# Performance work log

Hardware: AMD Instinct MI355X
Metric: run time of the kernel (lower is better)

Reference implementation:

```python
import jax, jax.numpy as jnp
import numpy as np


def setup_inputs() -> dict:
    key = jax.random.key(0)
    k1, k2, k3, k4 = jax.random.split(key, 4)
    B, D_vis, E, N = 512, 4096, 1024, 512
    vf = jax.random.normal(k1, (B, D_vis), dtype=jnp.float32)
    p_lfs = jax.random.normal(k2, (B, E), dtype=jnp.float32)
    n_lfs = jax.random.normal(k3, (N, E), dtype=jnp.float32)
    W = jax.random.normal(k4, (E, D_vis), dtype=jnp.float32) * (1.0 / np.sqrt(D_vis))
    b = jnp.zeros((E,), dtype=jnp.float32)
    return {"vf": vf, "p_lfs": p_lfs, "n_lfs": n_lfs, "W": W, "b": b}


def _partial_order_sim(hypers, hypos):
    # -||relu(hypers - hypos)||_2 along last dim
    act = jax.nn.relu(hypers - hypos)
    return -jnp.sqrt(jnp.sum(act * act, axis=-1))


def reference(vf, p_lfs, n_lfs, W, b):
    # vf: [B, D_vis], W: [E, D_vis] -> vf_emb: [B, E]
    vf_emb = jnp.einsum("bd,ed->be", vf, W) + b
    # positive scores: [B]
    p_scores = _partial_order_sim(p_lfs, vf_emb)
    # negative scores, batched over B: n_lfs [N,E] vs vf_emb [B,E] -> [B,N]
    n_scores = _partial_order_sim(n_lfs[None, :, :], vf_emb[:, None, :])
    # score_stack: [B, 1+N]
    return jnp.concatenate([p_scores[:, None], n_scores], axis=1)
```

## Files before the change

kernel.cpp:

```cpp
#include <hip/hip_runtime.h>
#include <hip/hip_bf16.h>

constexpr int B = 512;
constexpr int D = 4096;
constexpr int E = 1024;
constexpr int N = 512;
constexpr int KS = 16;
constexpr int KC = D / KS;
constexpr int NSTEP = KC / 32;
constexpr int ES = 8;
constexpr int EC = E / ES;
constexpr int DEPTH = 2;

typedef __attribute__((ext_vector_type(8))) short bf16x8;
typedef __attribute__((ext_vector_type(4))) float f32x4;
typedef _Float16 h2 __attribute__((ext_vector_type(2)));
typedef _Float16 h4 __attribute__((ext_vector_type(4)));
typedef _Float16 h8 __attribute__((ext_vector_type(8)));

typedef __attribute__((address_space(3))) void lds_void;
typedef const __attribute__((address_space(1))) void gbl_void;

__device__ __forceinline__ unsigned short f2bf(float f) {
    __hip_bfloat16 h = __float2bfloat16(f);
    return *reinterpret_cast<unsigned short*>(&h);
}

#if __has_builtin(__builtin_amdgcn_fdot2)
__device__ __forceinline__ float fdot2(h2 a, h2 b, float c) {
    return __builtin_amdgcn_fdot2(a, b, c, false);
}
#else
__device__ __forceinline__ float fdot2(h2 a, h2 b, float c) {
    return c + (float)a[0] * (float)b[0] + (float)a[1] * (float)b[1];
}
#endif

__global__ __launch_bounds__(256) void cvt_all(
    const float* __restrict__ vf, const float* __restrict__ W,
    const float* __restrict__ n_lfs,
    unsigned short* __restrict__ vfB, unsigned short* __restrict__ WB,
    _Float16* __restrict__ n16)
{
    const int bid = blockIdx.x;
    if (bid < 3072) {
        const float* src;
        unsigned short* dst;
        int i;
        if (bid < 1024) { src = vf; dst = vfB; i = (bid * 256 + threadIdx.x) * 8; }
        else           { src = W;  dst = WB;  i = ((bid - 1024) * 256 + threadIdx.x) * 8; }
        float4 v0 = *(const float4*)(src + i);
        float4 v1 = *(const float4*)(src + i + 4);
        bf16x8 o;
        o[0] = (short)f2bf(v0.x); o[1] = (short)f2bf(v0.y);
        o[2] = (short)f2bf(v0.z); o[3] = (short)f2bf(v0.w);
        o[4] = (short)f2bf(v1.x); o[5] = (short)f2bf(v1.y);
        o[6] = (short)f2bf(v1.z); o[7] = (short)f2bf(v1.w);
        *(bf16x8*)(dst + i) = o;
    } else {
        const int i = ((bid - 3072) * 256 + threadIdx.x) * 8;
        float4 v0 = *(const float4*)(n_lfs + i);
        float4 v1 = *(const float4*)(n_lfs + i + 4);
        h8 o;
        o[0] = (_Float16)v0.x; o[1] = (_Float16)v0.y;
        o[2] = (_Float16)v0.z; o[3] = (_Float16)v0.w;
        o[4] = (_Float16)v1.x; o[5] = (_Float16)v1.y;
        o[6] = (_Float16)v1.z; o[7] = (_Float16)v1.w;
        *(h8*)(n16 + i) = o;
    }
}

__global__ __launch_bounds__(64) void gemm_lds(
    const unsigned short* __restrict__ vf,
    const unsigned short* __restrict__ W,
    _Float16* __restrict__ part)
{
    __shared__ __align__(16) char smem[17664];

    const int L  = threadIdx.x;

    const int id = blockIdx.x + 16 * blockIdx.y + 128 * blockIdx.z;
    const int l  = (id & 7) * 256 + (id >> 3);
    const int ks = l >> 7;
    const int n0 = (l & 15) * 64;
    const int m0 = ((l >> 4) & 7) * 64;

    const int subrow = L >> 2;
    const int qstg = (L & 3) ^ ((L >> 2) & 3) ^ ((L >> 4) & 3);
    const int kbeg = ks * KC;
    const unsigned short* aSrc[4];
    const unsigned short* bSrc[4];
    #pragma unroll
    for (int c = 0; c < 4; ++c) {
        aSrc[c] = vf + (size_t)(m0 + c * 16 + subrow) * D + kbeg + qstg * 8;
        bSrc[c] = W  + (size_t)(n0 + c * 16 + subrow) * D + kbeg + qstg * 8;
    }

    const int r16 = L & 15;
    const int quad = L >> 4;
    const int swz = quad ^ (r16 & 3) ^ ((r16 >> 2) & 3);
    const int aoff = r16 * 64 + swz * 16;

    f32x4 acc[4][4] = {};

    auto issue = [&](int step, int buf) {
        const size_t koff = (size_t)step * 32;
        #pragma unroll
        for (int c = 0; c < 4; ++c) {
            __builtin_amdgcn_global_load_lds(
                (gbl_void*)(aSrc[c] + koff),
                (lds_void*)(smem + buf * 4096 + c * 1024), 16, 0, 0);
            __builtin_amdgcn_global_load_lds(
                (gbl_void*)(bSrc[c] + koff),
                (lds_void*)(smem + 8192 + buf * 4096 + c * 1024), 16, 0, 0);
        }
    };

    issue(0, 0);
    issue(1, 1);

    #define GSTEP(S, WC, ISS)                                                  \
    {                                                                          \
        const int buf_ = (S) & 1;                                              \
        __builtin_amdgcn_s_waitcnt(WC);                                        \
        bf16x8 af[4], bg[4];                                                   \
        _Pragma("unroll")                                                      \
        for (int i = 0; i < 4; ++i)                                            \
            af[i] = *(const bf16x8*)(smem + buf_ * 4096 + i * 1024 + aoff);    \
        _Pragma("unroll")                                                      \
        for (int j = 0; j < 4; ++j)                                            \
            bg[j] = *(const bf16x8*)(smem + 8192 + buf_ * 4096 + j * 1024 + aoff); \
        _Pragma("unroll")                                                      \
        for (int i = 0; i < 4; ++i)                                            \
            _Pragma("unroll")                                                  \
            for (int j = 0; j < 4; ++j)                                        \
                acc[i][j] = __builtin_amdgcn_mfma_f32_16x16x32_bf16(           \
                    af[i], bg[j], acc[i][j], 0, 0, 0);                         \
        if (ISS) issue((S) + DEPTH, buf_);                                     \
    }

    #pragma unroll 1
    for (int s = 0; s < NSTEP - 1; ++s)
        GSTEP(s, 0x0F78, s + DEPTH < NSTEP);
    GSTEP(NSTEP - 1, 0x0F70, false);
    #undef GSTEP

    float* ct = (float*)smem;
    #pragma unroll
    for (int i = 0; i < 4; ++i)
        #pragma unroll
        for (int j = 0; j < 4; ++j)
            #pragma unroll
            for (int r = 0; r < 4; ++r)
                ct[(i * 16 + quad * 4 + r) * 69 + (j * 16 + r16)] = acc[i][j][r];
    __builtin_amdgcn_s_waitcnt(0xC07F);
    __builtin_amdgcn_sched_barrier(0);
    _Float16* po = part + (size_t)ks * B * E + (size_t)(m0 + L) * E + n0;
    const float* crow = ct + L * 69;
    #pragma unroll
    for (int c8 = 0; c8 < 8; ++c8) {
        h8 v;
        #pragma unroll
        for (int u = 0; u < 8; ++u) v[u] = (_Float16)crow[c8 * 8 + u];
        *(h8*)(po + c8 * 8) = v;
    }
}

__global__ __launch_bounds__(256) void reduce_emb(
    const _Float16* __restrict__ part, const float* __restrict__ bias,
    const float* __restrict__ p_lfs,
    _Float16* __restrict__ emb16, float* __restrict__ out)
{
    const int b = blockIdx.x;
    const int e = threadIdx.x * 4;
    const size_t base = (size_t)b * E + e;
    float4 s = *(const float4*)(bias + e);
    #pragma unroll
    for (int ks = 0; ks < KS; ++ks) {
        h4 p = *(const h4*)(part + (size_t)ks * B * E + base);
        s.x += (float)p[0]; s.y += (float)p[1];
        s.z += (float)p[2]; s.w += (float)p[3];
    }
    h4 o;
    o[0] = (_Float16)s.x; o[1] = (_Float16)s.y;
    o[2] = (_Float16)s.z; o[3] = (_Float16)s.w;
    *(h4*)(emb16 + base) = o;

    const float4 pl = *(const float4*)(p_lfs + base);
    float d, a = 0.f;
    d = pl.x - s.x; d = fmaxf(d, 0.f); a = fmaf(d, d, a);
    d = pl.y - s.y; d = fmaxf(d, 0.f); a = fmaf(d, d, a);
    d = pl.z - s.z; d = fmaxf(d, 0.f); a = fmaf(d, d, a);
    d = pl.w - s.w; d = fmaxf(d, 0.f); a = fmaf(d, d, a);
    #pragma unroll
    for (int off = 32; off; off >>= 1) a += __shfl_down(a, off, 64);
    __shared__ float red[4];
    if ((threadIdx.x & 63) == 0) red[threadIdx.x >> 6] = a;
    __syncthreads();
    if (threadIdx.x == 0)
        out[(size_t)b * 513] = -sqrtf(red[0] + red[1] + red[2] + red[3]);
}

__global__ __launch_bounds__(256, 4) void scores_part(
    const _Float16* __restrict__ emb16,
    const _Float16* __restrict__ n16,
    _Float16* __restrict__ pn)
{
    constexpr int LDH = EC + 8;
    __shared__ _Float16 eS[64 * LDH];
    __shared__ _Float16 nS[64 * LDH];

    const int t  = threadIdx.x;
    const int n0 = blockIdx.x * 64;
    const int b0 = blockIdx.y * 64;
    const int e0 = blockIdx.z * EC;

    {
        const int row = t >> 2;
        const int cb  = (t & 3) * 32;
        const _Float16* ep = emb16 + (size_t)(b0 + row) * E + e0 + cb;
        const _Float16* np = n16   + (size_t)(n0 + row) * E + e0 + cb;
        _Float16* ed = &eS[row * LDH + cb];
        _Float16* nd = &nS[row * LDH + cb];
        #pragma unroll
        for (int q = 0; q < 4; ++q) {
            h8 v = *(const h8*)(ep + q * 8);
            h8 w = *(const h8*)(np + q * 8);
            *(h8*)(ed + q * 8) = -v;
            *(h8*)(nd + q * 8) = w;
        }
    }
    __syncthreads();

    const int ty = t >> 4;
    const int tx = t & 15;

    float acc[4][4] = {};
    const h4 z4 = {};

    #pragma unroll 2
    for (int e = 0; e < EC; e += 4) {
        h4 a[4], c[4];
        #pragma unroll
        for (int r = 0; r < 4; ++r)
            a[r] = *(const h4*)&eS[(ty + 16 * r) * LDH + e];
        #pragma unroll
        for (int q = 0; q < 4; ++q)
            c[q] = *(const h4*)&nS[(tx + 16 * q) * LDH + e];
        #pragma unroll
        for (int r = 0; r < 4; ++r)
            #pragma unroll
            for (int q = 0; q < 4; ++q) {
                h4 d = c[q] + a[r];
                d = __builtin_elementwise_max(d, z4);
                h2 dl = __builtin_shufflevector(d, d, 0, 1);
                h2 dh = __builtin_shufflevector(d, d, 2, 3);
                acc[r][q] = fdot2(dl, dl, acc[r][q]);
                acc[r][q] = fdot2(dh, dh, acc[r][q]);
            }
    }

    _Float16* po = pn + (size_t)blockIdx.z * B * N;
    #pragma unroll
    for (int r = 0; r < 4; ++r) {
        const size_t ob = (size_t)(b0 + ty + 16 * r) * N;
        #pragma unroll
        for (int q = 0; q < 4; ++q)
            po[ob + n0 + tx + 16 * q] = (_Float16)acc[r][q];
    }
}

__global__ __launch_bounds__(256) void scores_final(
    const _Float16* __restrict__ pn,
    float* __restrict__ out)
{
    const int i = blockIdx.x * 256 + threadIdx.x;
    const int b = i >> 9;
    const int n = i & (N - 1);
    float s = 0.f;
    #pragma unroll
    for (int z = 0; z < ES; ++z)
        s += (float)pn[(size_t)z * B * N + i];
    out[(size_t)b * 513 + 1 + n] = -sqrtf(s);
}

extern "C" void kernel_launch(void* const* d_in, const int* in_sizes, int n_in,
                              void* d_out, int out_size, void* d_ws, size_t ws_size,
                              hipStream_t stream) {
    const float* vf    = (const float*)d_in[0];
    const float* p_lfs = (const float*)d_in[1];
    const float* n_lfs = (const float*)d_in[2];
    const float* W     = (const float*)d_in[3];
    const float* bias  = (const float*)d_in[4];
    float* out = (float*)d_out;

    char* ws = (char*)d_ws;
    _Float16*       pg    = (_Float16*)ws;
    _Float16*       pn    = (_Float16*)ws;
    unsigned short* vfB   = (unsigned short*)(ws + ((size_t)16 << 20));
    unsigned short* WB    = (unsigned short*)(ws + ((size_t)20 << 20));
    _Float16*       emb16 = (_Float16*)(ws + ((size_t)28 << 20));
    _Float16*       n16   = (_Float16*)(ws + ((size_t)29 << 20));

    cvt_all<<<3328, 256, 0, stream>>>(vf, W, n_lfs, vfB, WB, n16);

    dim3 g1(E / 64, B / 64, KS);
    gemm_lds<<<g1, 64, 0, stream>>>(vfB, WB, pg);

    reduce_emb<<<B, 256, 0, stream>>>(pg, bias, p_lfs, emb16, out);

    dim3 g3(N / 64, B / 64, ES);
    scores_part<<<g3, 256, 0, stream>>>(emb16, n16, pn);

    scores_final<<<(B * N) / 256, 256, 0, stream>>>(pn, out);
}
```

Before: 118.2 us.

## Reduce split-K partials inside GEMM block across four waves

After: 113.4 us. -4.1%, faster.

```diff
diff --git a/kernel.cpp b/kernel.cpp
--- a/kernel.cpp
+++ b/kernel.cpp
@@ -5,8 +5,9 @@
 constexpr int D = 4096;
 constexpr int E = 1024;
 constexpr int N = 512;
-constexpr int KS = 16;
-constexpr int KC = D / KS;
+constexpr int KSW = 16;
+constexpr int KSG = 4;
+constexpr int KC = D / KSW;
 constexpr int NSTEP = KC / 32;
 constexpr int ES = 8;
 constexpr int EC = E / ES;
@@ -70,24 +71,28 @@
     }
 }
 
-__global__ __launch_bounds__(64) void gemm_lds(
+__global__ __launch_bounds__(256) void gemm_lds(
     const unsigned short* __restrict__ vf,
     const unsigned short* __restrict__ W,
     _Float16* __restrict__ part)
 {
-    __shared__ __align__(16) char smem[17664];
-
-    const int L  = threadIdx.x;
+    __shared__ __align__(16) char smem[70656];
+
+    const int t = threadIdx.x;
+    const int w = t >> 6;
+    const int L = t & 63;
 
     const int id = blockIdx.x + 16 * blockIdx.y + 128 * blockIdx.z;
-    const int l  = (id & 7) * 256 + (id >> 3);
-    const int ks = l >> 7;
+    const int l  = (id & 7) * 64 + (id >> 3);
+    const int z  = l >> 7;
     const int n0 = (l & 15) * 64;
     const int m0 = ((l >> 4) & 7) * 64;
 
+    char* stg = smem + w * 16384;
+
     const int subrow = L >> 2;
     const int qstg = (L & 3) ^ ((L >> 2) & 3) ^ ((L >> 4) & 3);
-    const int kbeg = ks * KC;
+    const int kbeg = (z * 4 + w) * KC;
     const unsigned short* aSrc[4];
     const unsigned short* bSrc[4];
     #pragma unroll
@@ -109,10 +114,10 @@
         for (int c = 0; c < 4; ++c) {
             __builtin_amdgcn_global_load_lds(
                 (gbl_void*)(aSrc[c] + koff),
-                (lds_void*)(smem + buf * 4096 + c * 1024), 16, 0, 0);
+                (lds_void*)(stg + buf * 4096 + c * 1024), 16, 0, 0);
             __builtin_amdgcn_global_load_lds(
                 (gbl_void*)(bSrc[c] + koff),
-                (lds_void*)(smem + 8192 + buf * 4096 + c * 1024), 16, 0, 0);
+                (lds_void*)(stg + 8192 + buf * 4096 + c * 1024), 16, 0, 0);
         }
     };
 
@@ -126,10 +131,10 @@
         bf16x8 af[4], bg[4];                                                   \
         _Pragma("unroll")                                                      \
         for (int i = 0; i < 4; ++i)                                            \
-            af[i] = *(const bf16x8*)(smem + buf_ * 4096 + i * 1024 + aoff);    \
+            af[i] = *(const bf16x8*)(stg + buf_ * 4096 + i * 1024 + aoff);     \
         _Pragma("unroll")                                                      \
         for (int j = 0; j < 4; ++j)                                            \
-            bg[j] = *(const bf16x8*)(smem + 8192 + buf_ * 4096 + j * 1024 + aoff); \
+            bg[j] = *(const bf16x8*)(stg + 8192 + buf_ * 4096 + j * 1024 + aoff); \
         _Pragma("unroll")                                                      \
         for (int i = 0; i < 4; ++i)                                            \
             _Pragma("unroll")                                                  \
@@ -145,25 +150,30 @@
     GSTEP(NSTEP - 1, 0x0F70, false);
     #undef GSTEP
 
-    float* ct = (float*)smem;
+    __syncthreads();
+    float* ctw = (float*)smem + w * 4416;
     #pragma unroll
     for (int i = 0; i < 4; ++i)
         #pragma unroll
         for (int j = 0; j < 4; ++j)
             #pragma unroll
             for (int r = 0; r < 4; ++r)
-                ct[(i * 16 + quad * 4 + r) * 69 + (j * 16 + r16)] = acc[i][j][r];
-    __builtin_amdgcn_s_waitcnt(0xC07F);
-    __builtin_amdgcn_sched_barrier(0);
-    _Float16* po = part + (size_t)ks * B * E + (size_t)(m0 + L) * E + n0;
-    const float* crow = ct + L * 69;
-    #pragma unroll
-    for (int c8 = 0; c8 < 8; ++c8) {
-        h8 v;
-        #pragma unroll
-        for (int u = 0; u < 8; ++u) v[u] = (_Float16)crow[c8 * 8 + u];
-        *(h8*)(po + c8 * 8) = v;
-    }
+                ctw[(i * 16 + quad * 4 + r) * 69 + (j * 16 + r16)] = acc[i][j][r];
+    __syncthreads();
+
+    const int row = t >> 2;
+    const int cb  = (t & 3) * 16;
+    const float* p0 = (const float*)smem + row * 69 + cb;
+    float s[16];
+    #pragma unroll
+    for (int u = 0; u < 16; ++u)
+        s[u] = (p0[u] + p0[4416 + u]) + (p0[8832 + u] + p0[13248 + u]);
+    _Float16* po = part + (size_t)z * B * E + (size_t)(m0 + row) * E + n0 + cb;
+    h8 v0, v1;
+    #pragma unroll
+    for (int u = 0; u < 8; ++u) { v0[u] = (_Float16)s[u]; v1[u] = (_Float16)s[u + 8]; }
+    *(h8*)po = v0;
+    *(h8*)(po + 8) = v1;
 }
 
 __global__ __launch_bounds__(256) void reduce_emb(
@@ -176,7 +186,7 @@
     const size_t base = (size_t)b * E + e;
     float4 s = *(const float4*)(bias + e);
     #pragma unroll
-    for (int ks = 0; ks < KS; ++ks) {
+    for (int ks = 0; ks < KSG; ++ks) {
         h4 p = *(const h4*)(part + (size_t)ks * B * E + base);
         s.x += (float)p[0]; s.y += (float)p[1];
         s.z += (float)p[2]; s.w += (float)p[3];
@@ -296,16 +306,16 @@
 
     char* ws = (char*)d_ws;
     _Float16*       pg    = (_Float16*)ws;
-    _Float16*       pn    = (_Float16*)ws;
-    unsigned short* vfB   = (unsigned short*)(ws + ((size_t)16 << 20));
-    unsigned short* WB    = (unsigned short*)(ws + ((size_t)20 << 20));
-    _Float16*       emb16 = (_Float16*)(ws + ((size_t)28 << 20));
-    _Float16*       n16   = (_Float16*)(ws + ((size_t)29 << 20));
+    _Float16*       pn    = (_Float16*)(ws + ((size_t)4 << 20));
+    unsigned short* vfB   = (unsigned short*)(ws + ((size_t)8 << 20));
+    unsigned short* WB    = (unsigned short*)(ws + ((size_t)12 << 20));
+    _Float16*       emb16 = (_Float16*)(ws + ((size_t)20 << 20));
+    _Float16*       n16   = (_Float16*)(ws + ((size_t)21 << 20));
 
     cvt_all<<<3328, 256, 0, stream>>>(vf, W, n_lfs, vfB, WB, n16);
 
-    dim3 g1(E / 64, B / 64, KS);
-    gemm_lds<<<g1, 64, 0, stream>>>(vfB, WB, pg);
+    dim3 g1(E / 64, B / 64, KSG);
+    gemm_lds<<<g1, 256, 0, stream>>>(vfB, WB, pg);
 
     reduce_emb<<<B, 256, 0, stream>>>(pg, bias, p_lfs, emb16, out);
 
```
